# Optimization experiments

Measured on AMD Instinct MI355X. Metric: run time of the kernel, lower is better.

Reference implementation:

```python
import jax, jax.numpy as jnp
import numpy as np

B, N = 8192, 4096
OUT_DIM = 32


def setup_inputs() -> dict:
    key = jax.random.key(0)
    k_rr, k_drop, k_w1, k_b1, k_w2, k_b2 = jax.random.split(key, 6)
    rr = jax.random.uniform(k_rr, (B, N), dtype=jnp.float32, minval=0.4, maxval=1.4)
    drop = jax.random.uniform(k_drop, (B, N)) < 0.3
    rr = jnp.where(drop, 0.0, rr)
    # projection MLP params (Linear(6,16) -> ReLU -> Dropout(eval: identity) -> Linear(16,32))
    w1 = jax.random.normal(k_w1, (6, 16), dtype=jnp.float32) * (1.0 / np.sqrt(6))
    b1 = jax.random.normal(k_b1, (16,), dtype=jnp.float32) * 0.01
    w2 = jax.random.normal(k_w2, (16, OUT_DIM), dtype=jnp.float32) * (1.0 / np.sqrt(16))
    b2 = jax.random.normal(k_b2, (OUT_DIM,), dtype=jnp.float32) * 0.01
    return {"rr_intervals": rr, "w1": w1, "b1": b1, "w2": w2, "b2": b2}


def _hrv_features(rr):
    # rr: (B, N) float32, zero-padded. Faithful to the per-row torch loop, vectorized.
    dt = rr.dtype
    mask = rr > 0                                   # (B, N)
    cnt = jnp.sum(mask, axis=1)                     # (B,) int
    cntf = cnt.astype(dt)
    # masked mean / unbiased std (torch.std default ddof=1)
    denom_m = jnp.maximum(cntf, 1.0)
    mean_rr = jnp.sum(jnp.where(mask, rr, 0.0), axis=1) / denom_m
    dev = jnp.where(mask, rr - mean_rr[:, None], 0.0)
    var = jnp.sum(dev * dev, axis=1) / jnp.maximum(cntf - 1.0, 1.0)
    sdnn = jnp.sqrt(var)
    # compact valid entries to the front (stable -> preserves order), so diffs
    # match torch.diff(rr[rr > 0])
    order = jnp.argsort(jnp.logical_not(mask), axis=1, stable=True)  # (B, N)
    compact = jnp.take_along_axis(rr, order, axis=1)                  # (B, N)
    diffs = compact[:, 1:] - compact[:, :-1]                          # (B, N-1)
    dmask = jnp.arange(N - 1)[None, :] < (cnt - 1)[:, None]           # valid diffs
    ndiff = jnp.maximum(cntf - 1.0, 1.0)
    rmssd = jnp.sqrt(jnp.sum(jnp.where(dmask, diffs * diffs, 0.0), axis=1) / ndiff)
    nn50 = jnp.sum(((jnp.abs(diffs) > 0.05) & dmask).astype(dt), axis=1)
    pnn50 = nn50 / ndiff
    hr = 60.0 / jnp.maximum(mean_rr, 1e-12)
    cv = sdnn / jnp.maximum(mean_rr, 1e-12)
    feats = jnp.stack([mean_rr, sdnn, rmssd, pnn50, hr, cv], axis=1)  # (B, 6)
    feats = jnp.where((cnt > 1)[:, None], feats, 0.0)
    # per-column batch normalization, applied only where column max > 0
    col_max = jnp.max(feats, axis=0)
    col_mean = jnp.mean(feats, axis=0)
    col_std = jnp.std(feats, axis=0, ddof=1)
    normed = (feats - col_mean[None, :]) / (col_std[None, :] + 1e-8)
    feats = jnp.where((col_max > 0)[None, :], normed, feats)
    return feats


def reference(rr_intervals, w1, b1, w2, b2):
    feats = _hrv_features(rr_intervals)                 # (B, 6)
    h = jax.nn.relu(feats @ w1 + b1)                    # (B, 16); dropout in eval = identity
    return h @ w2 + b2                                  # (B, OUT_DIM)
```

## Files before the change

kernel.cpp:

```cpp
#include <hip/hip_runtime.h>
#include <math.h>

#define BATCH 8192
#define NLEN 4096
#define THREADS 256
#define PER_THREAD (NLEN / THREADS)

__global__ __launch_bounds__(THREADS) void hrv_feats_kernel(
    const float* __restrict__ rr, float* __restrict__ feats) {
    __shared__ float sh_last[THREADS];
    __shared__ unsigned char sh_has[THREADS];
    __shared__ double sh_sum[4], sh_sumsq[4], sh_sumd2[4];
    __shared__ int sh_cnt[4], sh_nn50[4];

    const int row = blockIdx.x;
    const int t = threadIdx.x;
    const float* r = rr + (size_t)row * NLEN + t * PER_THREAD;

    float x[PER_THREAD];
    float4* xv = reinterpret_cast<float4*>(x);
    const float4* rv = reinterpret_cast<const float4*>(r);
#pragma unroll
    for (int i = 0; i < PER_THREAD / 4; ++i) xv[i] = rv[i];

    float sum = 0.f, sumsq = 0.f, sumd2 = 0.f;
    int cnt = 0, nn50 = 0;
    float first = 0.f, last = 0.f;
    int has = 0;
#pragma unroll
    for (int i = 0; i < PER_THREAD; ++i) {
        float v = x[i];
        if (v > 0.f) {
            sum += v;
            sumsq += v * v;
            ++cnt;
            if (has) {
                float d = v - last;
                sumd2 += d * d;
                nn50 += (fabsf(d) > 0.05f) ? 1 : 0;
            } else {
                first = v;
                has = 1;
            }
            last = v;
        }
    }
    sh_last[t] = last;
    sh_has[t] = (unsigned char)has;
    __syncthreads();
    if (has && t > 0) {
        for (int j = t - 1; j >= 0; --j) {
            if (sh_has[j]) {
                float d = first - sh_last[j];
                sumd2 += d * d;
                nn50 += (fabsf(d) > 0.05f) ? 1 : 0;
                break;
            }
        }
    }

    double dsum = sum, dsumsq = sumsq, dsumd2 = sumd2;
    int icnt = cnt, inn = nn50;
#pragma unroll
    for (int off = 32; off > 0; off >>= 1) {
        dsum += __shfl_down(dsum, off, 64);
        dsumsq += __shfl_down(dsumsq, off, 64);
        dsumd2 += __shfl_down(dsumd2, off, 64);
        icnt += __shfl_down(icnt, off, 64);
        inn += __shfl_down(inn, off, 64);
    }
    const int wave = t >> 6;
    if ((t & 63) == 0) {
        sh_sum[wave] = dsum;
        sh_sumsq[wave] = dsumsq;
        sh_sumd2[wave] = dsumd2;
        sh_cnt[wave] = icnt;
        sh_nn50[wave] = inn;
    }
    __syncthreads();
    if (t == 0) {
        double S = 0, S2 = 0, D2 = 0;
        int C = 0, NN = 0;
        for (int w = 0; w < 4; ++w) {
            S += sh_sum[w];
            S2 += sh_sumsq[w];
            D2 += sh_sumd2[w];
            C += sh_cnt[w];
            NN += sh_nn50[w];
        }
        const float cntf = (float)C;
        const float denom_m = fmaxf(cntf, 1.f);
        const float mean = (float)(S / (double)denom_m);
        const float varsum = (float)(S2 - (double)C * (double)mean * (double)mean);
        const float denom_v = fmaxf(cntf - 1.f, 1.f);
        const float sdnn = sqrtf(fmaxf(varsum / denom_v, 0.f));
        const float rmssd = sqrtf(fmaxf((float)(D2 / (double)denom_v), 0.f));
        const float pnn50 = (float)NN / denom_v;
        const float hr = 60.f / fmaxf(mean, 1e-12f);
        const float cv = sdnn / fmaxf(mean, 1e-12f);
        float f0 = mean, f1 = sdnn, f2 = rmssd, f3 = pnn50, f4 = hr, f5 = cv;
        if (C <= 1) { f0 = f1 = f2 = f3 = f4 = f5 = 0.f; }
        float* o = feats + row * 6;
        o[0] = f0; o[1] = f1; o[2] = f2;
        o[3] = f3; o[4] = f4; o[5] = f5;
    }
}

__global__ __launch_bounds__(THREADS) void col_stats_kernel(
    const float* __restrict__ feats, float* __restrict__ stats) {
    __shared__ double sh_s[4], sh_s2[4];
    __shared__ float sh_m[4];
    const int col = blockIdx.x;
    const int t = threadIdx.x;
    double s = 0.0, s2 = 0.0;
    float mx = -INFINITY;
    for (int i = t; i < BATCH; i += THREADS) {
        float f = feats[i * 6 + col];
        s += (double)f;
        s2 += (double)f * (double)f;
        mx = fmaxf(mx, f);
    }
#pragma unroll
    for (int off = 32; off > 0; off >>= 1) {
        s += __shfl_down(s, off, 64);
        s2 += __shfl_down(s2, off, 64);
        mx = fmaxf(mx, __shfl_down(mx, off, 64));
    }
    const int wave = t >> 6;
    if ((t & 63) == 0) { sh_s[wave] = s; sh_s2[wave] = s2; sh_m[wave] = mx; }
    __syncthreads();
    if (t == 0) {
        double S = 0, S2 = 0;
        float M = -INFINITY;
        for (int w = 0; w < 4; ++w) {
            S += sh_s[w];
            S2 += sh_s2[w];
            M = fmaxf(M, sh_m[w]);
        }
        const double meanb = S / (double)BATCH;
        double var = (S2 - (double)BATCH * meanb * meanb) / (double)(BATCH - 1);
        if (var < 0.0) var = 0.0;
        stats[col] = (float)meanb;
        stats[6 + col] = (float)sqrt(var);
        stats[12 + col] = M;
    }
}

__global__ __launch_bounds__(THREADS) void mlp_kernel(
    const float* __restrict__ feats, const float* __restrict__ stats,
    const float* __restrict__ w1, const float* __restrict__ b1,
    const float* __restrict__ w2, const float* __restrict__ b2,
    float* __restrict__ out) {
    const int tid = blockIdx.x * blockDim.x + threadIdx.x;
    if (tid >= BATCH) return;
    float f[6];
#pragma unroll
    for (int c = 0; c < 6; ++c) {
        float v = feats[tid * 6 + c];
        if (stats[12 + c] > 0.f) v = (v - stats[c]) / (stats[6 + c] + 1e-8f);
        f[c] = v;
    }
    float h[16];
#pragma unroll
    for (int j = 0; j < 16; ++j) {
        float a = b1[j];
#pragma unroll
        for (int c = 0; c < 6; ++c) a = fmaf(f[c], w1[c * 16 + j], a);
        h[j] = fmaxf(a, 0.f);
    }
    float o[32];
#pragma unroll
    for (int k = 0; k < 32; ++k) o[k] = b2[k];
#pragma unroll
    for (int j = 0; j < 16; ++j) {
        const float hj = h[j];
#pragma unroll
        for (int k = 0; k < 32; ++k) o[k] = fmaf(hj, w2[j * 32 + k], o[k]);
    }
    float4* ov = reinterpret_cast<float4*>(out + (size_t)tid * 32);
    const float4* op = reinterpret_cast<const float4*>(o);
#pragma unroll
    for (int i = 0; i < 8; ++i) ov[i] = op[i];
}

extern "C" void kernel_launch(void* const* d_in, const int* in_sizes, int n_in,
                              void* d_out, int out_size, void* d_ws, size_t ws_size,
                              hipStream_t stream) {
    const float* rr = (const float*)d_in[0];
    const float* w1 = (const float*)d_in[1];
    const float* b1 = (const float*)d_in[2];
    const float* w2 = (const float*)d_in[3];
    const float* b2 = (const float*)d_in[4];
    float* out = (float*)d_out;
    float* feats = (float*)d_ws;
    float* stats = feats + BATCH * 6;

    hrv_feats_kernel<<<BATCH, THREADS, 0, stream>>>(rr, feats);
    col_stats_kernel<<<6, THREADS, 0, stream>>>(feats, stats);
    mlp_kernel<<<BATCH / THREADS, THREADS, 0, stream>>>(feats, stats, w1, b1, w2, b2, out);
}
```

Measured before the change: 47.78 us.

## Map one wavefront per row and fuse column stats into MLP kernel

The feature kernel now gives each 64-lane wavefront one row, so each block covers four rows. The boundary-diff fixup uses a ballot and shuffle in place of shared memory and block barriers. The column-stats and MLP kernels are merged: every MLP block recomputes the six column statistics redundantly over all rows and keeps them in shared memory, which removes one launch and the tiny 6-block kernel. The cost is redundant reads of the feature buffer in each of the 32 blocks, and per-thread strided 64-element loads that coalesce less well.

```diff
diff --git a/kernel.cpp b/kernel.cpp
--- a/kernel.cpp
+++ b/kernel.cpp
@@ -3,161 +3,159 @@
 
 #define BATCH 8192
 #define NLEN 4096
-#define THREADS 256
-#define PER_THREAD (NLEN / THREADS)
 
-__global__ __launch_bounds__(THREADS) void hrv_feats_kernel(
+__global__ __launch_bounds__(256) void hrv_feats_kernel(
     const float* __restrict__ rr, float* __restrict__ feats) {
-    __shared__ float sh_last[THREADS];
-    __shared__ unsigned char sh_has[THREADS];
-    __shared__ double sh_sum[4], sh_sumsq[4], sh_sumd2[4];
-    __shared__ int sh_cnt[4], sh_nn50[4];
+    const int lane = threadIdx.x & 63;
+    const int wid = threadIdx.x >> 6;
+    const int row = blockIdx.x * 4 + wid;
+    const float* r = rr + (size_t)row * NLEN + lane * 64;
 
-    const int row = blockIdx.x;
-    const int t = threadIdx.x;
-    const float* r = rr + (size_t)row * NLEN + t * PER_THREAD;
+    double dsum = 0.0, dsumsq = 0.0, dsumd2 = 0.0;
+    int cnt = 0, nn50 = 0, has = 0;
+    float first = 0.f, last = 0.f;
 
-    float x[PER_THREAD];
+    float x[32];
     float4* xv = reinterpret_cast<float4*>(x);
     const float4* rv = reinterpret_cast<const float4*>(r);
+
 #pragma unroll
-    for (int i = 0; i < PER_THREAD / 4; ++i) xv[i] = rv[i];
-
-    float sum = 0.f, sumsq = 0.f, sumd2 = 0.f;
-    int cnt = 0, nn50 = 0;
-    float first = 0.f, last = 0.f;
-    int has = 0;
+    for (int half = 0; half < 2; ++half) {
 #pragma unroll
-    for (int i = 0; i < PER_THREAD; ++i) {
-        float v = x[i];
-        if (v > 0.f) {
-            sum += v;
-            sumsq += v * v;
-            ++cnt;
-            if (has) {
-                float d = v - last;
-                sumd2 += d * d;
-                nn50 += (fabsf(d) > 0.05f) ? 1 : 0;
-            } else {
-                first = v;
-                has = 1;
+        for (int i = 0; i < 8; ++i) xv[i] = rv[half * 8 + i];
+#pragma unroll
+        for (int c = 0; c < 2; ++c) {
+            float s = 0.f, s2 = 0.f, d2 = 0.f;
+#pragma unroll
+            for (int i = 0; i < 16; ++i) {
+                float v = x[c * 16 + i];
+                if (v > 0.f) {
+                    s += v;
+                    s2 += v * v;
+                    ++cnt;
+                    if (has) {
+                        float d = v - last;
+                        d2 += d * d;
+                        nn50 += (fabsf(d) > 0.05f) ? 1 : 0;
+                    } else {
+                        first = v;
+                        has = 1;
+                    }
+                    last = v;
+                }
             }
-            last = v;
-        }
-    }
-    sh_last[t] = last;
-    sh_has[t] = (unsigned char)has;
-    __syncthreads();
-    if (has && t > 0) {
-        for (int j = t - 1; j >= 0; --j) {
-            if (sh_has[j]) {
-                float d = first - sh_last[j];
-                sumd2 += d * d;
-                nn50 += (fabsf(d) > 0.05f) ? 1 : 0;
-                break;
-            }
+            dsum += s;
+            dsumsq += s2;
+            dsumd2 += d2;
         }
     }
 
-    double dsum = sum, dsumsq = sumsq, dsumd2 = sumd2;
-    int icnt = cnt, inn = nn50;
+    unsigned long long m = __ballot(has != 0);
+    unsigned long long pm = (lane == 0) ? 0ull : (m & ((1ull << lane) - 1ull));
+    int j = 63 - __clzll(pm | 1ull);
+    float lastj = __shfl(last, j, 64);
+    if (has && pm) {
+        float d = first - lastj;
+        dsumd2 += (double)(d * d);
+        nn50 += (fabsf(d) > 0.05f) ? 1 : 0;
+    }
+
 #pragma unroll
-    for (int off = 32; off > 0; off >>= 1) {
+    for (int off = 32; off; off >>= 1) {
         dsum += __shfl_down(dsum, off, 64);
         dsumsq += __shfl_down(dsumsq, off, 64);
         dsumd2 += __shfl_down(dsumd2, off, 64);
-        icnt += __shfl_down(icnt, off, 64);
-        inn += __shfl_down(inn, off, 64);
+        cnt += __shfl_down(cnt, off, 64);
+        nn50 += __shfl_down(nn50, off, 64);
     }
-    const int wave = t >> 6;
-    if ((t & 63) == 0) {
-        sh_sum[wave] = dsum;
-        sh_sumsq[wave] = dsumsq;
-        sh_sumd2[wave] = dsumd2;
-        sh_cnt[wave] = icnt;
-        sh_nn50[wave] = inn;
-    }
-    __syncthreads();
-    if (t == 0) {
-        double S = 0, S2 = 0, D2 = 0;
-        int C = 0, NN = 0;
-        for (int w = 0; w < 4; ++w) {
-            S += sh_sum[w];
-            S2 += sh_sumsq[w];
-            D2 += sh_sumd2[w];
-            C += sh_cnt[w];
-            NN += sh_nn50[w];
-        }
-        const float cntf = (float)C;
+
+    if (lane == 0) {
+        const float cntf = (float)cnt;
         const float denom_m = fmaxf(cntf, 1.f);
-        const float mean = (float)(S / (double)denom_m);
-        const float varsum = (float)(S2 - (double)C * (double)mean * (double)mean);
+        const float mean = (float)(dsum / (double)denom_m);
+        const float varsum = (float)(dsumsq - (double)cnt * (double)mean * (double)mean);
         const float denom_v = fmaxf(cntf - 1.f, 1.f);
         const float sdnn = sqrtf(fmaxf(varsum / denom_v, 0.f));
-        const float rmssd = sqrtf(fmaxf((float)(D2 / (double)denom_v), 0.f));
-        const float pnn50 = (float)NN / denom_v;
+        const float rmssd = sqrtf(fmaxf((float)(dsumd2 / (double)denom_v), 0.f));
+        const float pnn50 = (float)nn50 / denom_v;
         const float hr = 60.f / fmaxf(mean, 1e-12f);
         const float cv = sdnn / fmaxf(mean, 1e-12f);
         float f0 = mean, f1 = sdnn, f2 = rmssd, f3 = pnn50, f4 = hr, f5 = cv;
-        if (C <= 1) { f0 = f1 = f2 = f3 = f4 = f5 = 0.f; }
+        if (cnt <= 1) { f0 = f1 = f2 = f3 = f4 = f5 = 0.f; }
         float* o = feats + row * 6;
         o[0] = f0; o[1] = f1; o[2] = f2;
         o[3] = f3; o[4] = f4; o[5] = f5;
     }
 }
 
-__global__ __launch_bounds__(THREADS) void col_stats_kernel(
-    const float* __restrict__ feats, float* __restrict__ stats) {
-    __shared__ double sh_s[4], sh_s2[4];
-    __shared__ float sh_m[4];
-    const int col = blockIdx.x;
+__global__ __launch_bounds__(256) void stats_mlp_kernel(
+    const float* __restrict__ feats,
+    const float* __restrict__ w1, const float* __restrict__ b1,
+    const float* __restrict__ w2, const float* __restrict__ b2,
+    float* __restrict__ out) {
+    __shared__ double sh_s[4][6], sh_s2[4][6];
+    __shared__ float sh_m[4][6];
+    __shared__ float sh_stats[18];
+
     const int t = threadIdx.x;
-    double s = 0.0, s2 = 0.0;
-    float mx = -INFINITY;
-    for (int i = t; i < BATCH; i += THREADS) {
-        float f = feats[i * 6 + col];
-        s += (double)f;
-        s2 += (double)f * (double)f;
-        mx = fmaxf(mx, f);
+    double s[6] = {0, 0, 0, 0, 0, 0};
+    double s2[6] = {0, 0, 0, 0, 0, 0};
+    float mx[6] = {-INFINITY, -INFINITY, -INFINITY, -INFINITY, -INFINITY, -INFINITY};
+
+#pragma unroll 4
+    for (int i = t; i < BATCH; i += 256) {
+        const float* fp = feats + i * 6;
+#pragma unroll
+        for (int c = 0; c < 6; ++c) {
+            float f = fp[c];
+            s[c] += (double)f;
+            s2[c] += (double)f * (double)f;
+            mx[c] = fmaxf(mx[c], f);
+        }
     }
 #pragma unroll
-    for (int off = 32; off > 0; off >>= 1) {
-        s += __shfl_down(s, off, 64);
-        s2 += __shfl_down(s2, off, 64);
-        mx = fmaxf(mx, __shfl_down(mx, off, 64));
+    for (int off = 32; off; off >>= 1) {
+#pragma unroll
+        for (int c = 0; c < 6; ++c) {
+            s[c] += __shfl_down(s[c], off, 64);
+            s2[c] += __shfl_down(s2[c], off, 64);
+            mx[c] = fmaxf(mx[c], __shfl_down(mx[c], off, 64));
+        }
     }
-    const int wave = t >> 6;
-    if ((t & 63) == 0) { sh_s[wave] = s; sh_s2[wave] = s2; sh_m[wave] = mx; }
+    if ((t & 63) == 0) {
+        const int w = t >> 6;
+#pragma unroll
+        for (int c = 0; c < 6; ++c) {
+            sh_s[w][c] = s[c];
+            sh_s2[w][c] = s2[c];
+            sh_m[w][c] = mx[c];
+        }
+    }
     __syncthreads();
-    if (t == 0) {
+    if (t < 6) {
         double S = 0, S2 = 0;
         float M = -INFINITY;
         for (int w = 0; w < 4; ++w) {
-            S += sh_s[w];
-            S2 += sh_s2[w];
-            M = fmaxf(M, sh_m[w]);
+            S += sh_s[w][t];
+            S2 += sh_s2[w][t];
+            M = fmaxf(M, sh_m[w][t]);
         }
         const double meanb = S / (double)BATCH;
         double var = (S2 - (double)BATCH * meanb * meanb) / (double)(BATCH - 1);
         if (var < 0.0) var = 0.0;
-        stats[col] = (float)meanb;
-        stats[6 + col] = (float)sqrt(var);
-        stats[12 + col] = M;
+        sh_stats[t] = (float)meanb;
+        sh_stats[6 + t] = (float)sqrt(var);
+        sh_stats[12 + t] = M;
     }
-}
+    __syncthreads();
 
-__global__ __launch_bounds__(THREADS) void mlp_kernel(
-    const float* __restrict__ feats, const float* __restrict__ stats,
-    const float* __restrict__ w1, const float* __restrict__ b1,
-    const float* __restrict__ w2, const float* __restrict__ b2,
-    float* __restrict__ out) {
-    const int tid = blockIdx.x * blockDim.x + threadIdx.x;
-    if (tid >= BATCH) return;
+    const int row = blockIdx.x * 256 + t;
+    const float* fp = feats + row * 6;
     float f[6];
 #pragma unroll
     for (int c = 0; c < 6; ++c) {
-        float v = feats[tid * 6 + c];
-        if (stats[12 + c] > 0.f) v = (v - stats[c]) / (stats[6 + c] + 1e-8f);
+        float v = fp[c];
+        if (sh_stats[12 + c] > 0.f) v = (v - sh_stats[c]) / (sh_stats[6 + c] + 1e-8f);
         f[c] = v;
     }
     float h[16];
@@ -177,7 +175,7 @@
 #pragma unroll
         for (int k = 0; k < 32; ++k) o[k] = fmaf(hj, w2[j * 32 + k], o[k]);
     }
-    float4* ov = reinterpret_cast<float4*>(out + (size_t)tid * 32);
+    float4* ov = reinterpret_cast<float4*>(out + (size_t)row * 32);
     const float4* op = reinterpret_cast<const float4*>(o);
 #pragma unroll
     for (int i = 0; i < 8; ++i) ov[i] = op[i];
@@ -193,9 +191,7 @@
     const float* b2 = (const float*)d_in[4];
     float* out = (float*)d_out;
     float* feats = (float*)d_ws;
-    float* stats = feats + BATCH * 6;
 
-    hrv_feats_kernel<<<BATCH, THREADS, 0, stream>>>(rr, feats);
-    col_stats_kernel<<<6, THREADS, 0, stream>>>(feats, stats);
-    mlp_kernel<<<BATCH / THREADS, THREADS, 0, stream>>>(feats, stats, w1, b1, w2, b2, out);
+    hrv_feats_kernel<<<BATCH / 4, 256, 0, stream>>>(rr, feats);
+    stats_mlp_kernel<<<BATCH / 256, 256, 0, stream>>>(feats, w1, b1, w2, b2, out);
 }
```

New measurement: 41.59 us. 1.15x faster.
